# Optimization experiments

Hardware: AMD Instinct MI355X
Metric: run time of the kernel (lower is better)

Reference implementation:

```python
import jax, jax.numpy as jnp
import numpy as np

N_TASK = 50000
N_EDGE = 50000
E = 500000
F_TASK = 64
F_EDGE = 64
H = 256
OUT = 256


def _lin(key, fan_in, fan_out):
    kw, kb = jax.random.split(key)
    lim = 1.0 / np.sqrt(fan_in)
    W = jax.random.uniform(kw, (fan_in, fan_out), minval=-lim, maxval=lim, dtype=jnp.float32)
    b = jax.random.uniform(kb, (fan_out,), minval=-lim, maxval=lim, dtype=jnp.float32)
    return W, b


def setup_inputs() -> dict:
    key = jax.random.key(0)
    ks = jax.random.split(key, 20)
    inp = {}
    inp['task_features'] = jax.random.normal(ks[0], (N_TASK, F_TASK), dtype=jnp.float32)
    inp['edge_features'] = jax.random.normal(ks[1], (N_EDGE, F_EDGE), dtype=jnp.float32)
    inp['queue_edges'] = jax.random.randint(ks[2], (2, E), 0, N_TASK)
    inp['type_edges'] = jax.random.randint(ks[3], (2, E), 0, N_TASK)
    inp['affinity_edges'] = jax.random.randint(ks[4], (2, E), 0, N_TASK)  # src<num_tasks, tgt<num_edges
    inp['topology_edges'] = jax.random.randint(ks[5], (2, E), 0, N_EDGE)
    inp['te_w1'], inp['te_b1'] = _lin(ks[6], F_TASK, H)
    inp['te_w2'], inp['te_b2'] = _lin(ks[7], H, H)
    inp['ee_w1'], inp['ee_b1'] = _lin(ks[8], F_EDGE, H)
    inp['ee_w2'], inp['ee_b2'] = _lin(ks[9], H, H)
    inp['gnn_w0'], inp['gnn_b0'] = _lin(ks[10], H, H)
    inp['gnn_w1'], inp['gnn_b1'] = _lin(ks[11], H, H)
    inp['ta_w'], inp['ta_b'] = _lin(ks[12], H, H)
    inp['ea_w'], inp['ea_b'] = _lin(ks[13], H, H)
    inp['out_w1'], inp['out_b1'] = _lin(ks[14], 2 * H, H)
    inp['out_w2'], inp['out_b2'] = _lin(ks[15], H, OUT)
    return inp


def _mean_msg(src_emb, src, tgt, num_segments):
    # scatter-add messages from src nodes into tgt slots, divide by in-degree (clamped >=1)
    msgs = jax.ops.segment_sum(src_emb[src], tgt, num_segments=num_segments)
    cnt = jax.ops.segment_sum(jnp.ones_like(src, dtype=src_emb.dtype), tgt, num_segments=num_segments)
    return msgs / jnp.maximum(cnt, 1.0)[:, None]


def _forward(task_features, edge_features, queue_edges, type_edges, affinity_edges, topology_edges,
             te_w1, te_b1, te_w2, te_b2, ee_w1, ee_b1, ee_w2, ee_b2,
             gnn_w0, gnn_b0, gnn_w1, gnn_b1, ta_w, ta_b, ea_w, ea_b,
             out_w1, out_b1, out_w2, out_b2):
    relu = jax.nn.relu
    # node encoders (Linear-ReLU-Linear-ReLU)
    t = relu(relu(task_features @ te_w1 + te_b1) @ te_w2 + te_b2)   # [N_task, H]
    e = relu(relu(edge_features @ ee_w1 + ee_b1) @ ee_w2 + ee_b2)   # [N_edge, H]

    # queue convolution: messages computed ONCE from original t (torch code never updates task_embeddings in loop)
    qs, qt = queue_edges[0], queue_edges[1]
    q_msgs = jax.ops.segment_sum(t[qs], qt, num_segments=t.shape[0])
    h = t
    for W, b in ((gnn_w0, gnn_b0), (gnn_w1, gnn_b1)):
        h = relu((h + 0.5 * q_msgs) @ W + b)
    t = h

    # type convolution: mean-aggregated same-type messages
    t = t + 0.3 * _mean_msg(t, type_edges[0], type_edges[1], t.shape[0])

    # affinity convolution: bipartite task<->edge exchange (simultaneous update)
    asrc, atgt = affinity_edges[0], affinity_edges[1]
    t_msgs = jax.ops.segment_sum(e[atgt], asrc, num_segments=t.shape[0])
    t_cnt = jax.ops.segment_sum(jnp.ones((asrc.shape[0],), t.dtype), asrc, num_segments=t.shape[0])
    e_msgs = jax.ops.segment_sum(t[asrc], atgt, num_segments=e.shape[0])
    e_cnt = jax.ops.segment_sum(jnp.ones((atgt.shape[0],), e.dtype), atgt, num_segments=e.shape[0])
    t_new = t + 0.3 * t_msgs / jnp.maximum(t_cnt, 1.0)[:, None]
    e_new = e + 0.3 * e_msgs / jnp.maximum(e_cnt, 1.0)[:, None]
    t, e = t_new, e_new

    # topology convolution: edge-edge mean aggregation
    e = e + 0.3 * _mean_msg(e, topology_edges[0], topology_edges[1], e.shape[0])

    # graph-level aggregation
    t_agg = relu(jnp.mean(t, axis=0) @ ta_w + ta_b)  # [H]
    e_agg = relu(jnp.mean(e, axis=0) @ ea_w + ea_b)  # [H]
    combined = jnp.concatenate([t_agg, e_agg], axis=0)  # [2H]
    out = relu(combined @ out_w1 + out_b1) @ out_w2 + out_b2  # [OUT]
    return out


def reference(task_features, edge_features, queue_edges, type_edges, affinity_edges, topology_edges,
              te_w1, te_b1, te_w2, te_b2, ee_w1, ee_b1, ee_w2, ee_b2,
              gnn_w0, gnn_b0, gnn_w1, gnn_b1, ta_w, ta_b, ea_w, ea_b,
              out_w1, out_b1, out_w2, out_b2):
    return _forward(task_features, edge_features, queue_edges, type_edges, affinity_edges, topology_edges,
                    te_w1, te_b1, te_w2, te_b2, ee_w1, ee_b1, ee_w2, ee_b2,
                    gnn_w0, gnn_b0, gnn_w1, gnn_b1, ta_w, ta_b, ea_w, ea_b,
                    out_w1, out_b1, out_w2, out_b2)
```

## Files before the change

### kernel.cpp

```cpp
#include <hip/hip_runtime.h>

#define H 256
#define NT 50000
#define NEDGE 50000
#define NE 500000

#define NBKT 391
#define NBLK 123
#define CHUNK 4096
#define CAP 2816

typedef __attribute__((ext_vector_type(8))) short short8_t;
typedef __attribute__((ext_vector_type(4))) float f32x4;
typedef unsigned short u16;
typedef unsigned int u32;

__device__ __forceinline__ void fatomic(float* p, float v) { unsafeAtomicAdd(p, v); }

__device__ __forceinline__ float b2f(u16 v) { return __uint_as_float((u32)v << 16); }
__device__ __forceinline__ u16 f2b(float f) {
    u32 u = __float_as_uint(f);
    u += 0x7FFFu + ((u >> 16) & 1u);
    return (u16)(u >> 16);
}

__device__ __forceinline__ u32 f2fp8_1(float f) {
    u32 u = __float_as_uint(f);
    u32 s = (u >> 24) & 0x80u;
    float af = fabsf(f);
    if (af >= 448.f) return s | 0x7Eu;
    if (af < 0.015625f) {
        int m = (int)rintf(af * 512.0f);
        return s | (u32)m;
    }
    u32 au = __float_as_uint(af);
    u32 r = au + 0x7FFFFu + ((au >> 20) & 1u);
    int e = (int)(r >> 23) - 127;
    return s | (u32)(((e + 7) << 3) | ((r >> 20) & 7u));
}
__device__ __forceinline__ float fp82f_1(u32 b) {
    u32 s = (b & 0x80u) << 24;
    u32 em = b & 0x7Fu;
    float v;
    if (em >= 8) v = __uint_as_float((((em >> 3) + 120u) << 23) | ((em & 7u) << 20));
    else v = (float)em * 0.001953125f;
    return __uint_as_float(__float_as_uint(v) | s);
}
__device__ __forceinline__ u32 pk4_fp8(float a, float b, float c, float d) {
#if __has_builtin(__builtin_amdgcn_cvt_pk_fp8_f32)
    u32 r = 0;
    r = (u32)__builtin_amdgcn_cvt_pk_fp8_f32(a, b, (int)r, false);
    r = (u32)__builtin_amdgcn_cvt_pk_fp8_f32(c, d, (int)r, true);
    return r;
#else
    return f2fp8_1(a) | (f2fp8_1(b) << 8) | (f2fp8_1(c) << 16) | (f2fp8_1(d) << 24);
#endif
}
__device__ __forceinline__ float4 unpk4_fp8(u32 v) {
#if __has_builtin(__builtin_amdgcn_cvt_pk_f32_fp8)
    auto lo = __builtin_amdgcn_cvt_pk_f32_fp8(v, false);
    auto hi = __builtin_amdgcn_cvt_pk_f32_fp8(v, true);
    return make_float4(lo[0], lo[1], hi[0], hi[1]);
#else
    return make_float4(fp82f_1(v & 255u), fp82f_1((v >> 8) & 255u),
                       fp82f_1((v >> 16) & 255u), fp82f_1(v >> 24));
#endif
}

__device__ __forceinline__ const int* pick_list(
    int l, const int* a, const int* b, const int* c, const int* d, const int* e)
{ return (l == 0) ? a : (l == 1) ? b : (l == 2) ? c : (l == 3) ? d : e; }

template<int K1, bool FUSE_Q, bool XF32, bool DUAL>
__global__ __launch_bounds__(256) void fused_mlp(
    const void* __restrict__ XA, const u16* __restrict__ Q,
    const u16* __restrict__ W1hA, const u16* __restrict__ W1lA, const float* __restrict__ b1A,
    const u16* __restrict__ W2hA, const u16* __restrict__ W2lA, const float* __restrict__ b2A,
    u16* __restrict__ outA, u32* __restrict__ f8A,
    const void* __restrict__ XB,
    const u16* __restrict__ W1hB, const u16* __restrict__ W1lB, const float* __restrict__ b1B,
    const u16* __restrict__ W2hB, const u16* __restrict__ W2lB, const float* __restrict__ b2B,
    u16* __restrict__ outB, u32* __restrict__ f8B,
    int N, int nA, float s2)
{
    __shared__ u16 lds[32 * 256];
    int bid = blockIdx.x;
    const void* X = XA;
    const u16 *W1h = W1hA, *W1l = W1lA, *W2h = W2hA, *W2l = W2lA;
    const float *b1 = b1A, *b2 = b2A;
    u16* out = outA;
    u32* f8 = f8A;
    if (DUAL && bid >= nA) {
        bid -= nA; X = XB;
        W1h = W1hB; W1l = W1lB; b1 = b1B;
        W2h = W2hB; W2l = W2lB; b2 = b2B;
        out = outB; f8 = f8B;
    }
    const int m0 = bid * 32;

    constexpr int RCH = K1 / 8;
    for (int i = threadIdx.x; i < 32 * RCH; i += 256) {
        int r = i / RCH, c8 = i % RCH;
        int gr = m0 + r; if (gr >= N) gr = N - 1;
        uint4 v;
        if (XF32) {
            const float* xf = (const float*)X + (size_t)gr * K1 + c8 * 8;
            float4 a = *(const float4*)xf;
            float4 b = *(const float4*)(xf + 4);
            v.x = (u32)f2b(a.x) | ((u32)f2b(a.y) << 16);
            v.y = (u32)f2b(a.z) | ((u32)f2b(a.w) << 16);
            v.z = (u32)f2b(b.x) | ((u32)f2b(b.y) << 16);
            v.w = (u32)f2b(b.z) | ((u32)f2b(b.w) << 16);
        } else {
            v = *(const uint4*)((const u16*)X + (size_t)gr * K1 + c8 * 8);
        }
        u32 byte = (u32)(r * (K1 * 2) + c8 * 16) ^ (u32)((r & 7) << 4);
        *(uint4*)((char*)lds + byte) = v;
    }
    __syncthreads();

    const int wv = threadIdx.x >> 6, l = threadIdx.x & 63;
    const int li = l & 15, lk = l >> 4;

    f32x4 acc[2][4];
    #pragma unroll
    for (int i = 0; i < 2; i++)
        #pragma unroll
        for (int j = 0; j < 4; j++)
            acc[i][j] = (f32x4){0.f, 0.f, 0.f, 0.f};

    {
        constexpr int KS = K1 / 32;
        short8_t whc[4], wlc[4];
        #pragma unroll
        for (int ni = 0; ni < 4; ni++) {
            const size_t wi = (size_t)((wv * 4 + ni) * KS) * 64 + l;
            whc[ni] = ((const short8_t*)W1h)[wi];
            wlc[ni] = ((const short8_t*)W1l)[wi];
        }
        #pragma unroll
        for (int ks = 0; ks < KS; ks++) {
            short8_t whn[4], wln[4];
            if (ks + 1 < KS) {
                #pragma unroll
                for (int ni = 0; ni < 4; ni++) {
                    const size_t wi = (size_t)((wv * 4 + ni) * KS + ks + 1) * 64 + l;
                    whn[ni] = ((const short8_t*)W1h)[wi];
                    wln[ni] = ((const short8_t*)W1l)[wi];
                }
            }
            short8_t xb[2];
            #pragma unroll
            for (int mi = 0; mi < 2; mi++) {
                int m = mi * 16 + li;
                u32 byte = (u32)(m * (K1 * 2) + (ks * 32 + lk * 8) * 2) ^ (u32)((m & 7) << 4);
                xb[mi] = *(const short8_t*)((const char*)lds + byte);
            }
            __builtin_amdgcn_s_setprio(1);
            #pragma unroll
            for (int ni = 0; ni < 4; ni++)
                #pragma unroll
                for (int mi = 0; mi < 2; mi++) {
                    acc[mi][ni] = __builtin_amdgcn_mfma_f32_16x16x32_bf16(wlc[ni], xb[mi], acc[mi][ni], 0, 0, 0);
                    acc[mi][ni] = __builtin_amdgcn_mfma_f32_16x16x32_bf16(whc[ni], xb[mi], acc[mi][ni], 0, 0, 0);
                }
            __builtin_amdgcn_s_setprio(0);
            if (ks + 1 < KS) {
                #pragma unroll
                for (int ni = 0; ni < 4; ni++) { whc[ni] = whn[ni]; wlc[ni] = wln[ni]; }
            }
        }
    }

    __syncthreads();

    #pragma unroll
    for (int ni = 0; ni < 4; ni++) {
        int c = wv * 64 + ni * 16 + lk * 4;
        float4 b4 = *(const float4*)(b1 + c);
        #pragma unroll
        for (int mi = 0; mi < 2; mi++) {
            int m = mi * 16 + li;
            float o0 = fmaxf(acc[mi][ni][0] + b4.x, 0.f);
            float o1 = fmaxf(acc[mi][ni][1] + b4.y, 0.f);
            float o2 = fmaxf(acc[mi][ni][2] + b4.z, 0.f);
            float o3 = fmaxf(acc[mi][ni][3] + b4.w, 0.f);
            if (FUSE_Q) {
                int gm = m0 + m; if (gm >= N) gm = N - 1;
                uint2 qv = *(const uint2*)(Q + (size_t)gm * 256 + c);
                o0 = fmaf(s2, b2f((u16)(qv.x & 0xFFFF)), o0);
                o1 = fmaf(s2, b2f((u16)(qv.x >> 16)), o1);
                o2 = fmaf(s2, b2f((u16)(qv.y & 0xFFFF)), o2);
                o3 = fmaf(s2, b2f((u16)(qv.y >> 16)), o3);
            }
            u32 w0 = (u32)f2b(o0) | ((u32)f2b(o1) << 16);
            u32 w1 = (u32)f2b(o2) | ((u32)f2b(o3) << 16);
            u32 byte = (u32)(m * 512 + c * 2) ^ (u32)((m & 7) << 4);
            *(uint2*)((char*)lds + byte) = make_uint2(w0, w1);
        }
    }
    __syncthreads();

    #pragma unroll
    for (int i = 0; i < 2; i++)
        #pragma unroll
        for (int j = 0; j < 4; j++)
            acc[i][j] = (f32x4){0.f, 0.f, 0.f, 0.f};

    {
        short8_t whc[4], wlc[4];
        #pragma unroll
        for (int ni = 0; ni < 4; ni++) {
            const size_t wi = (size_t)((wv * 4 + ni) * 8) * 64 + l;
            whc[ni] = ((const short8_t*)W2h)[wi];
            wlc[ni] = ((const short8_t*)W2l)[wi];
        }
        #pragma unroll
        for (int ks = 0; ks < 8; ks++) {
            short8_t whn[4], wln[4];
            if (ks + 1 < 8) {
                #pragma unroll
                for (int ni = 0; ni < 4; ni++) {
                    const size_t wi = (size_t)((wv * 4 + ni) * 8 + ks + 1) * 64 + l;
                    whn[ni] = ((const short8_t*)W2h)[wi];
                    wln[ni] = ((const short8_t*)W2l)[wi];
                }
            }
            short8_t xb[2];
            #pragma unroll
            for (int mi = 0; mi < 2; mi++) {
                int m = mi * 16 + li;
                u32 byte = (u32)(m * 512 + (ks * 32 + lk * 8) * 2) ^ (u32)((m & 7) << 4);
                xb[mi] = *(const short8_t*)((const char*)lds + byte);
            }
            __builtin_amdgcn_s_setprio(1);
            #pragma unroll
            for (int ni = 0; ni < 4; ni++)
                #pragma unroll
                for (int mi = 0; mi < 2; mi++) {
                    acc[mi][ni] = __builtin_amdgcn_mfma_f32_16x16x32_bf16(wlc[ni], xb[mi], acc[mi][ni], 0, 0, 0);
                    acc[mi][ni] = __builtin_amdgcn_mfma_f32_16x16x32_bf16(whc[ni], xb[mi], acc[mi][ni], 0, 0, 0);
                }
            __builtin_amdgcn_s_setprio(0);
            if (ks + 1 < 8) {
                #pragma unroll
                for (int ni = 0; ni < 4; ni++) { whc[ni] = whn[ni]; wlc[ni] = wln[ni]; }
            }
        }
    }

    #pragma unroll
    for (int mi = 0; mi < 2; mi++) {
        int m = m0 + mi * 16 + li;
        if (m < N) {
            #pragma unroll
            for (int ni = 0; ni < 4; ni++) {
                int c = wv * 64 + ni * 16 + lk * 4;
                float4 b4 = *(const float4*)(b2 + c);
                float o0 = fmaxf(acc[mi][ni][0] + b4.x, 0.f);
                float o1 = fmaxf(acc[mi][ni][1] + b4.y, 0.f);
                float o2 = fmaxf(acc[mi][ni][2] + b4.z, 0.f);
                float o3 = fmaxf(acc[mi][ni][3] + b4.w, 0.f);
                u32 w0 = (u32)f2b(o0) | ((u32)f2b(o1) << 16);
                u32 w1 = (u32)f2b(o2) | ((u32)f2b(o3) << 16);
                *(uint2*)(out + (size_t)m * H + c) = make_uint2(w0, w1);
                if (f8) f8[(size_t)m * 64 + (c >> 2)] = pk4_fp8(o0, o1, o2, o3);
            }
        }
    }
}

__global__ __launch_bounds__(256) void wt_pack(
    const float* __restrict__ s0, const float* __restrict__ s1,
    const float* __restrict__ s2, const float* __restrict__ s3,
    const float* __restrict__ s4, const float* __restrict__ s5,
    u16* __restrict__ arena)
{
    const int li = blockIdx.y;
    const int K = (li == 0 || li == 4) ? 64 : 256;
    const int offs[6] = {0, 32768, 163840, 294912, 425984, 458752};
    int n = K * 256;
    int i = blockIdx.x * 256 + threadIdx.x;
    if (i >= n) return;
    const float* W = (li == 0) ? s0 : (li == 1) ? s1 : (li == 2) ? s2
                   : (li == 3) ? s3 : (li == 4) ? s4 : s5;
    u16* hi = arena + offs[li];
    u16* lo = hi + n;
    int k = i >> 8, c = i & 255;
    float u = W[i];
    u32 b = __float_as_uint(u);
    float r = u - __uint_as_float(b & 0xFFFF0000u);
    int lane = ((k >> 3) & 3) * 16 + (c & 15);
    size_t idx = ((size_t)((c >> 4) * (K >> 5) + (k >> 5)) * 64 + lane) * 8 + (k & 7);
    hi[idx] = (u16)(b >> 16);
    lo[idx] = f2b(r);
}

__global__ __launch_bounds__(256) void hist_kernel(
    const int* __restrict__ k0, const int* __restrict__ k1, const int* __restrict__ k2,
// ... 117 lines not shown
    int base = bases[l * (NBKT + 1) + b];
    int end  = bases[l * (NBKT + 1) + b + 1];
    int sz = end - base; if (sz > CAP) sz = CAP;
    int* c = csr + (size_t)l * NE;
    for (int i = t; i < sz; i += 256) seg[i] = c[base + i];
    if (t < 128) hist[t] = 0;
    __syncthreads();
    for (int i = t; i < sz; i += 256) atomicAdd(&hist[seg[i] >> 16], 1);
    __syncthreads();
    if (t < 128) scn[t] = hist[t];
    __syncthreads();
    for (int st = 1; st < 128; st <<= 1) {
        int v = 0;
        if (t < 128 && t >= st) v = scn[t - st];
        __syncthreads();
        if (t < 128) scn[t] += v;
        __syncthreads();
    }
    if (t < 128) {
        int key = b * 128 + t;
        int excl = scn[t] - hist[t];
        if (key < NT) off[l * (NT + 1) + key] = base + excl;
        hist[t] = excl;
    }
    if (b == 0 && t == 128) off[l * (NT + 1) + NT] = NE;
    __syncthreads();
    for (int i = t; i < sz; i += 256) {
        int u = seg[i];
        int p = atomicAdd(&hist[u >> 16], 1);
        c[base + p] = u & 0xFFFF;
    }
}

__global__ __launch_bounds__(256) void gather_q_f8(
    const u32* __restrict__ src, const int* __restrict__ csr,
    const int* __restrict__ off, const u16* __restrict__ baseT,
    u16* __restrict__ sumOut, u16* __restrict__ fuseOut, float s2, int N)
{
    int r = (blockIdx.x * 256 + threadIdx.x) >> 6;
    int lane = threadIdx.x & 63;
    if (r >= N) return;
    int o0 = off[r];
    int d  = off[r + 1] - o0;
    float4 acc = {0.f, 0.f, 0.f, 0.f};
    int j = 0;
    for (; j + 8 <= d; j += 8) {
        u32 w[8];
        #pragma unroll
        for (int q = 0; q < 8; q++)
            w[q] = src[(size_t)csr[o0 + j + q] * 64 + lane];
        #pragma unroll
        for (int q = 0; q < 8; q++) {
            float4 f = unpk4_fp8(w[q]);
            acc.x += f.x; acc.y += f.y; acc.z += f.z; acc.w += f.w;
        }
    }
    for (; j < d; j++) {
        float4 f = unpk4_fp8(src[(size_t)csr[o0 + j] * 64 + lane]);
        acc.x += f.x; acc.y += f.y; acc.z += f.z; acc.w += f.w;
    }
    ushort4 pk;
    pk.x = f2b(acc.x); pk.y = f2b(acc.y); pk.z = f2b(acc.z); pk.w = f2b(acc.w);
    ((ushort4*)(sumOut + (size_t)r * H))[lane] = pk;
    ushort4 b = ((const ushort4*)(baseT + (size_t)r * H))[lane];
    pk.x = f2b(fmaf(s2, acc.x, b2f(b.x)));
    pk.y = f2b(fmaf(s2, acc.y, b2f(b.y)));
    pk.z = f2b(fmaf(s2, acc.z, b2f(b.z)));
    pk.w = f2b(fmaf(s2, acc.w, b2f(b.w)));
    ((ushort4*)(fuseOut + (size_t)r * H))[lane] = pk;
}

__global__ __launch_bounds__(256) void gather_mean_f8(
    const u32* __restrict__ srcA, const int* __restrict__ csrA, const int* __restrict__ offA,
    const u16* __restrict__ baseA, u16* __restrict__ dstA, u32* __restrict__ m8A,
    const u32* __restrict__ srcB, const int* __restrict__ csrB, const int* __restrict__ offB,
    const u16* __restrict__ baseB, u16* __restrict__ dstB, u32* __restrict__ m8B,
    float alpha, int nA, int N)
{
    int bid = blockIdx.x;
    const u32* src = srcA; const int* csr = csrA; const int* off = offA;
    const u16* base = baseA; u16* dst = dstA; u32* m8 = m8A;
    if (bid >= nA) {
        bid -= nA; src = srcB; csr = csrB; off = offB; base = baseB; dst = dstB; m8 = m8B;
    }
    int r = (bid * 256 + threadIdx.x) >> 6;
    int lane = threadIdx.x & 63;
    if (r >= N) return;
    int o0 = off[r];
    int d  = off[r + 1] - o0;
    float4 acc = {0.f, 0.f, 0.f, 0.f};
    int j = 0;
    for (; j + 8 <= d; j += 8) {
        u32 w[8];
        #pragma unroll
        for (int q = 0; q < 8; q++)
            w[q] = src[(size_t)csr[o0 + j + q] * 64 + lane];
        #pragma unroll
        for (int q = 0; q < 8; q++) {
            float4 f = unpk4_fp8(w[q]);
            acc.x += f.x; acc.y += f.y; acc.z += f.z; acc.w += f.w;
        }
    }
    for (; j < d; j++) {
        float4 f = unpk4_fp8(src[(size_t)csr[o0 + j] * 64 + lane]);
        acc.x += f.x; acc.y += f.y; acc.z += f.z; acc.w += f.w;
    }
    float s = alpha / (float)max(d, 1);
    ushort4 b = ((const ushort4*)(base + (size_t)r * H))[lane];
    float o0f = fmaf(s, acc.x, b2f(b.x));
    float o1f = fmaf(s, acc.y, b2f(b.y));
    float o2f = fmaf(s, acc.z, b2f(b.z));
    float o3f = fmaf(s, acc.w, b2f(b.w));
    ushort4 pk;
    pk.x = f2b(o0f); pk.y = f2b(o1f); pk.z = f2b(o2f); pk.w = f2b(o3f);
    ((ushort4*)(dst + (size_t)r * H))[lane] = pk;
    if (m8) m8[(size_t)r * 64 + lane] = pk4_fp8(o0f, o1f, o2f, o3f);
}

__global__ __launch_bounds__(256) void colsum2(
    const u16* __restrict__ embA, float* __restrict__ accA,
    const u16* __restrict__ embB, float* __restrict__ accB, int N)
{
    const u16* emb = embA; float* acc = accA;
    int blk = blockIdx.x;
    if (blk >= 256) { blk -= 256; emb = embB; acc = accB; }
    int c = threadIdx.x;
    float s = 0.f;
    for (int r = blk; r < N; r += 256)
        s += b2f(emb[(size_t)r * H + c]);
    fatomic(&acc[c], s);
}

__global__ __launch_bounds__(256) void final_mlp(
    const float* __restrict__ sumT, const float* __restrict__ sumE,
    float invNT, float invNE,
    const float* __restrict__ ta_w, const float* __restrict__ ta_b,
    const float* __restrict__ ea_w, const float* __restrict__ ea_b,
    const float* __restrict__ ow1, const float* __restrict__ ob1,
    const float* __restrict__ ow2, const float* __restrict__ ob2,
    float* __restrict__ out)
{
    __shared__ float tm[H], em[H], comb[2 * H], hid[H];
    int t = threadIdx.x;
    tm[t] = sumT[t] * invNT;
    em[t] = sumE[t] * invNE;
    __syncthreads();
    float s = ta_b[t];
    for (int k = 0; k < H; k++) s += tm[k] * ta_w[k * H + t];
    comb[t] = fmaxf(s, 0.f);
    s = ea_b[t];
    for (int k = 0; k < H; k++) s += em[k] * ea_w[k * H + t];
    comb[H + t] = fmaxf(s, 0.f);
    __syncthreads();
    s = ob1[t];
    for (int k = 0; k < 2 * H; k++) s += comb[k] * ow1[k * H + t];
    hid[t] = fmaxf(s, 0.f);
    __syncthreads();
    s = ob2[t];
    for (int k = 0; k < H; k++) s += hid[k] * ow2[k * H + t];
    out[t] = s;
}

extern "C" void kernel_launch(void* const* d_in, const int* in_sizes, int n_in,
                              void* d_out, int out_size, void* d_ws, size_t ws_size,
                              hipStream_t stream) {
    const float* tf  = (const float*)d_in[0];
    const float* ef  = (const float*)d_in[1];
    const int*   qe  = (const int*)d_in[2];
    const int*   te  = (const int*)d_in[3];
    const int*   ae  = (const int*)d_in[4];
    const int*   pe  = (const int*)d_in[5];
    const float* te_w1 = (const float*)d_in[6];  const float* te_b1 = (const float*)d_in[7];
    const float* te_w2 = (const float*)d_in[8];  const float* te_b2 = (const float*)d_in[9];
    const float* ee_w1 = (const float*)d_in[10]; const float* ee_b1 = (const float*)d_in[11];
    const float* ee_w2 = (const float*)d_in[12]; const float* ee_b2 = (const float*)d_in[13];
    const float* gw0 = (const float*)d_in[14];   const float* gb0 = (const float*)d_in[15];
    const float* gw1 = (const float*)d_in[16];   const float* gb1 = (const float*)d_in[17];
    const float* ta_w = (const float*)d_in[18];  const float* ta_b = (const float*)d_in[19];
    const float* ea_w = (const float*)d_in[20];  const float* ea_b = (const float*)d_in[21];
    const float* ow1 = (const float*)d_in[22];   const float* ob1 = (const float*)d_in[23];
    const float* ow2 = (const float*)d_in[24];   const float* ob2 = (const float*)d_in[25];

    const size_t NB = (size_t)NT * H;
    u16* T  = (u16*)d_ws;
    u16* Bf = T + NB;
    u16* S  = Bf + NB;
    u16* F  = S + NB;
    float* sumT = (float*)(F + NB);
    float* sumE = sumT + H;
    int* off5   = (int*)(sumE + H);
    int* csr5   = off5 + 5 * (NT + 1);
    int* counts = csr5 + (size_t)5 * NE;
    int* starts = counts + (size_t)5 * NBLK * NBKT;
    int* bases  = starts + (size_t)5 * NBLK * NBKT;
    u16* arena = (u16*)(((size_t)counts + 15) & ~(size_t)15);
    u16* wt_te1_h = arena + 0;      u16* wt_te1_l = arena + 16384;
    u16* wt_te2_h = arena + 32768;  u16* wt_te2_l = arena + 98304;
    u16* wt_g0_h  = arena + 163840; u16* wt_g0_l  = arena + 229376;
    u16* wt_g1_h  = arena + 294912; u16* wt_g1_l  = arena + 360448;
    u16* wt_ee1_h = arena + 425984; u16* wt_ee1_l = arena + 442368;
    u16* wt_ee2_h = arena + 458752; u16* wt_ee2_l = arena + 524288;
    u32* M0 = (u32*)(((size_t)(bases + 5 * (NBKT + 1)) + 15) & ~(size_t)15);
    u32* M1 = M0 + NB / 4;
    u32* M2 = M1 + NB / 4;
    u32* M3 = M2 + NB / 4;
    u32* M4 = M3 + NB / 4;

    const int MGR = (NT + 31) / 32;
    const int GB = (NT * 64) / 256;

    const int *k0 = qe + NE, *k1 = te + NE, *k2 = ae,      *k3 = ae + NE, *k4 = pe + NE;
    const int *v0 = qe,      *v1 = te,      *v2 = ae + NE, *v3 = ae,      *v4 = pe;

    dim3 pg(NBLK, 5);
    hist_kernel<<<pg, 256, 0, stream>>>(k0, k1, k2, k3, k4, counts);
    scan_buckets<<<5, 256, 0, stream>>>(counts, starts, bases);
    partition_kernel<<<pg, 256, 0, stream>>>(k0, k1, k2, k3, k4, v0, v1, v2, v3, v4,
                                             starts, csr5);
    wt_pack<<<dim3(256, 6), 256, 0, stream>>>(te_w1, te_w2, gw0, gw1, ee_w1, ee_w2, arena);
    bucket_csr<<<dim3(NBKT, 5), 256, 0, stream>>>(bases, csr5, off5);

    #define LOFF(l) (off5 + (l) * (NT + 1))
    #define LCSR(l) (csr5 + (size_t)(l) * NE)

    fused_mlp<64, false, true, true><<<2 * MGR, 256, 0, stream>>>(
        tf, nullptr, wt_te1_h, wt_te1_l, te_b1, wt_te2_h, wt_te2_l, te_b2, T, M0,
        ef, wt_ee1_h, wt_ee1_l, ee_b1, wt_ee2_h, wt_ee2_l, ee_b2, Bf, M2,
        NT, MGR, 0.f);

    gather_q_f8<<<GB, 256, 0, stream>>>(M0, LCSR(0), LOFF(0), T, S, F, 0.5f, NT);

    fused_mlp<256, true, false, false><<<MGR, 256, 0, stream>>>(
        F, S, wt_g0_h, wt_g0_l, gb0, wt_g1_h, wt_g1_l, gb1, T, M1,
        nullptr, nullptr, nullptr, nullptr, nullptr, nullptr, nullptr, nullptr, nullptr,
        NT, MGR, 0.5f);

    gather_mean_f8<<<GB, 256, 0, stream>>>(
        M1, LCSR(1), LOFF(1), T, F, M3,
        M1, LCSR(1), LOFF(1), T, F, M3,
        0.3f, GB, NT);

    gather_mean_f8<<<2 * GB, 256, 0, stream>>>(
        M2, LCSR(2), LOFF(2), F, S, nullptr,
        M3, LCSR(3), LOFF(3), Bf, T, M4,
        0.3f, GB, NT);

    gather_mean_f8<<<GB, 256, 0, stream>>>(
        M4, LCSR(4), LOFF(4), T, Bf, nullptr,
        M4, LCSR(4), LOFF(4), T, Bf, nullptr,
        0.3f, GB, NT);

    hipMemsetAsync(sumT, 0, H * 4, stream);
    hipMemsetAsync(sumE, 0, H * 4, stream);
    colsum2<<<512, 256, 0, stream>>>(S, sumT, Bf, sumE, NT);
    final_mlp<<<1, 256, 0, stream>>>(sumT, sumE, 1.f / NT, 1.f / NEDGE,
                                     ta_w, ta_b, ea_w, ea_b, ow1, ob1, ow2, ob2,
                                     (float*)d_out);
}
```

Measured before the change: 465.1 us.

## Fuse queue gather into GNN MLP kernel, widen MLP tiles to 64 rows

The separate queue-edge gather kernel is folded into a new gnn_fused kernel. It aggregates fp8 neighbour messages straight into LDS and then runs both GNN linear layers, so the S and F intermediates no longer make a round trip through global memory. The fused MLP kernels now process 64 rows per block instead of 32, which doubles register accumulators and LDS use in exchange for more weight reuse. The column-sum reduction drops its memsets and atomics and writes per-block partials that final_mlp reduces serially. The risks are lower occupancy from 64 KB of LDS in gnn_fused and a serial 256-step loop in the single-block final kernel.

Measured after the change: 497.6 us. +7.0%, slower.

```diff
diff --git a/kernel.cpp b/kernel.cpp
--- a/kernel.cpp
+++ b/kernel.cpp
@@ -14,8 +14,6 @@
 typedef __attribute__((ext_vector_type(4))) float f32x4;
 typedef unsigned short u16;
 typedef unsigned int u32;
-
-__device__ __forceinline__ void fatomic(float* p, float v) { unsafeAtomicAdd(p, v); }
 
 __device__ __forceinline__ float b2f(u16 v) { return __uint_as_float((u32)v << 16); }
 __device__ __forceinline__ u16 f2b(float f) {
@@ -71,9 +69,9 @@
     int l, const int* a, const int* b, const int* c, const int* d, const int* e)
 { return (l == 0) ? a : (l == 1) ? b : (l == 2) ? c : (l == 3) ? d : e; }
 
-template<int K1, bool FUSE_Q, bool XF32, bool DUAL>
+template<int K1, bool XF32, bool DUAL>
 __global__ __launch_bounds__(256) void fused_mlp(
-    const void* __restrict__ XA, const u16* __restrict__ Q,
+    const void* __restrict__ XA,
     const u16* __restrict__ W1hA, const u16* __restrict__ W1lA, const float* __restrict__ b1A,
     const u16* __restrict__ W2hA, const u16* __restrict__ W2lA, const float* __restrict__ b2A,
     u16* __restrict__ outA, u32* __restrict__ f8A,
@@ -81,9 +79,9 @@
     const u16* __restrict__ W1hB, const u16* __restrict__ W1lB, const float* __restrict__ b1B,
     const u16* __restrict__ W2hB, const u16* __restrict__ W2lB, const float* __restrict__ b2B,
     u16* __restrict__ outB, u32* __restrict__ f8B,
-    int N, int nA, float s2)
-{
-    __shared__ u16 lds[32 * 256];
+    int N, int nA)
+{
+    __shared__ u16 lds[64 * 256];
     int bid = blockIdx.x;
     const void* X = XA;
     const u16 *W1h = W1hA, *W1l = W1lA, *W2h = W2hA, *W2l = W2lA;
@@ -96,10 +94,10 @@
         W2h = W2hB; W2l = W2lB; b2 = b2B;
         out = outB; f8 = f8B;
     }
-    const int m0 = bid * 32;
+    const int m0 = bid * 64;
 
     constexpr int RCH = K1 / 8;
-    for (int i = threadIdx.x; i < 32 * RCH; i += 256) {
+    for (int i = threadIdx.x; i < 64 * RCH; i += 256) {
         int r = i / RCH, c8 = i % RCH;
         int gr = m0 + r; if (gr >= N) gr = N - 1;
         uint4 v;
@@ -122,9 +120,9 @@
     const int wv = threadIdx.x >> 6, l = threadIdx.x & 63;
     const int li = l & 15, lk = l >> 4;
 
-    f32x4 acc[2][4];
-    #pragma unroll
-    for (int i = 0; i < 2; i++)
+    f32x4 acc[4][4];
+    #pragma unroll
+    for (int i = 0; i < 4; i++)
         #pragma unroll
         for (int j = 0; j < 4; j++)
             acc[i][j] = (f32x4){0.f, 0.f, 0.f, 0.f};
@@ -149,9 +147,9 @@
                     wln[ni] = ((const short8_t*)W1l)[wi];
                 }
             }
-            short8_t xb[2];
-            #pragma unroll
-            for (int mi = 0; mi < 2; mi++) {
+            short8_t xb[4];
+            #pragma unroll
+            for (int mi = 0; mi < 4; mi++) {
                 int m = mi * 16 + li;
                 u32 byte = (u32)(m * (K1 * 2) + (ks * 32 + lk * 8) * 2) ^ (u32)((m & 7) << 4);
                 xb[mi] = *(const short8_t*)((const char*)lds + byte);
@@ -160,7 +158,7 @@
             #pragma unroll
             for (int ni = 0; ni < 4; ni++)
                 #pragma unroll
-                for (int mi = 0; mi < 2; mi++) {
+                for (int mi = 0; mi < 4; mi++) {
                     acc[mi][ni] = __builtin_amdgcn_mfma_f32_16x16x32_bf16(wlc[ni], xb[mi], acc[mi][ni], 0, 0, 0);
                     acc[mi][ni] = __builtin_amdgcn_mfma_f32_16x16x32_bf16(whc[ni], xb[mi], acc[mi][ni], 0, 0, 0);
                 }
@@ -179,20 +177,12 @@
         int c = wv * 64 + ni * 16 + lk * 4;
         float4 b4 = *(const float4*)(b1 + c);
         #pragma unroll
-        for (int mi = 0; mi < 2; mi++) {
+        for (int mi = 0; mi < 4; mi++) {
             int m = mi * 16 + li;
             float o0 = fmaxf(acc[mi][ni][0] + b4.x, 0.f);
             float o1 = fmaxf(acc[mi][ni][1] + b4.y, 0.f);
             float o2 = fmaxf(acc[mi][ni][2] + b4.z, 0.f);
             float o3 = fmaxf(acc[mi][ni][3] + b4.w, 0.f);
-            if (FUSE_Q) {
-                int gm = m0 + m; if (gm >= N) gm = N - 1;
-                uint2 qv = *(const uint2*)(Q + (size_t)gm * 256 + c);
-                o0 = fmaf(s2, b2f((u16)(qv.x & 0xFFFF)), o0);
-                o1 = fmaf(s2, b2f((u16)(qv.x >> 16)), o1);
-                o2 = fmaf(s2, b2f((u16)(qv.y & 0xFFFF)), o2);
-                o3 = fmaf(s2, b2f((u16)(qv.y >> 16)), o3);
-            }
             u32 w0 = (u32)f2b(o0) | ((u32)f2b(o1) << 16);
             u32 w1 = (u32)f2b(o2) | ((u32)f2b(o3) << 16);
             u32 byte = (u32)(m * 512 + c * 2) ^ (u32)((m & 7) << 4);
@@ -202,7 +192,7 @@
     __syncthreads();
 
     #pragma unroll
-    for (int i = 0; i < 2; i++)
+    for (int i = 0; i < 4; i++)
         #pragma unroll
         for (int j = 0; j < 4; j++)
             acc[i][j] = (f32x4){0.f, 0.f, 0.f, 0.f};
@@ -226,9 +216,9 @@
                     wln[ni] = ((const short8_t*)W2l)[wi];
                 }
             }
-            short8_t xb[2];
-            #pragma unroll
-            for (int mi = 0; mi < 2; mi++) {
+            short8_t xb[4];
+            #pragma unroll
+            for (int mi = 0; mi < 4; mi++) {
                 int m = mi * 16 + li;
                 u32 byte = (u32)(m * 512 + (ks * 32 + lk * 8) * 2) ^ (u32)((m & 7) << 4);
                 xb[mi] = *(const short8_t*)((const char*)lds + byte);
@@ -237,7 +227,7 @@
             #pragma unroll
             for (int ni = 0; ni < 4; ni++)
                 #pragma unroll
-                for (int mi = 0; mi < 2; mi++) {
+                for (int mi = 0; mi < 4; mi++) {
                     acc[mi][ni] = __builtin_amdgcn_mfma_f32_16x16x32_bf16(wlc[ni], xb[mi], acc[mi][ni], 0, 0, 0);
                     acc[mi][ni] = __builtin_amdgcn_mfma_f32_16x16x32_bf16(whc[ni], xb[mi], acc[mi][ni], 0, 0, 0);
                 }
@@ -250,7 +240,199 @@
     }
 
     #pragma unroll
-    for (int mi = 0; mi < 2; mi++) {
+    for (int mi = 0; mi < 4; mi++) {
+        int m = m0 + mi * 16 + li;
+        if (m < N) {
+            #pragma unroll
+            for (int ni = 0; ni < 4; ni++) {
+                int c = wv * 64 + ni * 16 + lk * 4;
+                float4 b4 = *(const float4*)(b2 + c);
+                float o0 = fmaxf(acc[mi][ni][0] + b4.x, 0.f);
+                float o1 = fmaxf(acc[mi][ni][1] + b4.y, 0.f);
+                float o2 = fmaxf(acc[mi][ni][2] + b4.z, 0.f);
+                float o3 = fmaxf(acc[mi][ni][3] + b4.w, 0.f);
+                u32 w0 = (u32)f2b(o0) | ((u32)f2b(o1) << 16);
+                u32 w1 = (u32)f2b(o2) | ((u32)f2b(o3) << 16);
+                *(uint2*)(out + (size_t)m * H + c) = make_uint2(w0, w1);
+                if (f8) f8[(size_t)m * 64 + (c >> 2)] = pk4_fp8(o0, o1, o2, o3);
+            }
+        }
+    }
+}
+
+__global__ __launch_bounds__(256) void gnn_fused(
+    const u16* __restrict__ T, const u32* __restrict__ M0,
+    const int* __restrict__ csr, const int* __restrict__ off,
+    const u16* __restrict__ W1h, const u16* __restrict__ W1l, const float* __restrict__ b1,
+    const u16* __restrict__ W2h, const u16* __restrict__ W2l, const float* __restrict__ b2,
+    u16* __restrict__ out, u32* __restrict__ f8, int N)
+{
+    __shared__ u16 ldsX[64 * 256];
+    __shared__ u16 ldsS[64 * 256];
+    const int wv = threadIdx.x >> 6, l = threadIdx.x & 63;
+    const int li = l & 15, lk = l >> 4;
+    const int m0 = blockIdx.x * 64;
+
+    for (int rr = 0; rr < 16; rr++) {
+        int r = wv * 16 + rr;
+        int gr = m0 + r; if (gr >= N) gr = N - 1;
+        int o0 = off[gr];
+        int d  = off[gr + 1] - o0;
+        float4 acc = {0.f, 0.f, 0.f, 0.f};
+        int j = 0;
+        for (; j + 8 <= d; j += 8) {
+            u32 w[8];
+            #pragma unroll
+            for (int q = 0; q < 8; q++)
+                w[q] = M0[(size_t)csr[o0 + j + q] * 64 + l];
+            #pragma unroll
+            for (int q = 0; q < 8; q++) {
+                float4 f = unpk4_fp8(w[q]);
+                acc.x += f.x; acc.y += f.y; acc.z += f.z; acc.w += f.w;
+            }
+        }
+        for (; j < d; j++) {
+            float4 f = unpk4_fp8(M0[(size_t)csr[o0 + j] * 64 + l]);
+            acc.x += f.x; acc.y += f.y; acc.z += f.z; acc.w += f.w;
+        }
+        ushort4 t4 = ((const ushort4*)(T + (size_t)gr * H))[l];
+        u32 s0 = (u32)f2b(acc.x) | ((u32)f2b(acc.y) << 16);
+        u32 s1 = (u32)f2b(acc.z) | ((u32)f2b(acc.w) << 16);
+        u32 f0 = (u32)f2b(fmaf(0.5f, acc.x, b2f(t4.x)))
+               | ((u32)f2b(fmaf(0.5f, acc.y, b2f(t4.y))) << 16);
+        u32 f1 = (u32)f2b(fmaf(0.5f, acc.z, b2f(t4.z)))
+               | ((u32)f2b(fmaf(0.5f, acc.w, b2f(t4.w))) << 16);
+        u32 byte = (u32)(r * 512 + l * 8) ^ (u32)((r & 7) << 4);
+        *(uint2*)((char*)ldsX + byte) = make_uint2(f0, f1);
+        *(uint2*)((char*)ldsS + byte) = make_uint2(s0, s1);
+    }
+    __syncthreads();
+
+    f32x4 acc[4][4];
+    #pragma unroll
+    for (int i = 0; i < 4; i++)
+        #pragma unroll
+        for (int j = 0; j < 4; j++)
+            acc[i][j] = (f32x4){0.f, 0.f, 0.f, 0.f};
+
+    {
+        short8_t whc[4], wlc[4];
+        #pragma unroll
+        for (int ni = 0; ni < 4; ni++) {
+            const size_t wi = (size_t)((wv * 4 + ni) * 8) * 64 + l;
+            whc[ni] = ((const short8_t*)W1h)[wi];
+            wlc[ni] = ((const short8_t*)W1l)[wi];
+        }
+        #pragma unroll
+        for (int ks = 0; ks < 8; ks++) {
+            short8_t whn[4], wln[4];
+            if (ks + 1 < 8) {
+                #pragma unroll
+                for (int ni = 0; ni < 4; ni++) {
+                    const size_t wi = (size_t)((wv * 4 + ni) * 8 + ks + 1) * 64 + l;
+                    whn[ni] = ((const short8_t*)W1h)[wi];
+                    wln[ni] = ((const short8_t*)W1l)[wi];
+                }
+            }
+            short8_t xb[4];
+            #pragma unroll
+            for (int mi = 0; mi < 4; mi++) {
+                int m = mi * 16 + li;
+                u32 byte = (u32)(m * 512 + (ks * 32 + lk * 8) * 2) ^ (u32)((m & 7) << 4);
+                xb[mi] = *(const short8_t*)((const char*)ldsX + byte);
+            }
+            __builtin_amdgcn_s_setprio(1);
+            #pragma unroll
+            for (int ni = 0; ni < 4; ni++)
+                #pragma unroll
+                for (int mi = 0; mi < 4; mi++) {
+                    acc[mi][ni] = __builtin_amdgcn_mfma_f32_16x16x32_bf16(wlc[ni], xb[mi], acc[mi][ni], 0, 0, 0);
+                    acc[mi][ni] = __builtin_amdgcn_mfma_f32_16x16x32_bf16(whc[ni], xb[mi], acc[mi][ni], 0, 0, 0);
+                }
+            __builtin_amdgcn_s_setprio(0);
+            if (ks + 1 < 8) {
+                #pragma unroll
+                for (int ni = 0; ni < 4; ni++) { whc[ni] = whn[ni]; wlc[ni] = wln[ni]; }
+            }
+        }
+    }
+
+    __syncthreads();
+
+    #pragma unroll
+    for (int ni = 0; ni < 4; ni++) {
+        int c = wv * 64 + ni * 16 + lk * 4;
+        float4 b4 = *(const float4*)(b1 + c);
+        #pragma unroll
+        for (int mi = 0; mi < 4; mi++) {
+            int m = mi * 16 + li;
+            u32 byte = (u32)(m * 512 + c * 2) ^ (u32)((m & 7) << 4);
+            uint2 sv = *(const uint2*)((const char*)ldsS + byte);
+            float o0 = fmaxf(acc[mi][ni][0] + b4.x, 0.f);
+            float o1 = fmaxf(acc[mi][ni][1] + b4.y, 0.f);
+            float o2 = fmaxf(acc[mi][ni][2] + b4.z, 0.f);
+            float o3 = fmaxf(acc[mi][ni][3] + b4.w, 0.f);
+            o0 = fmaf(0.5f, b2f((u16)(sv.x & 0xFFFF)), o0);
+            o1 = fmaf(0.5f, b2f((u16)(sv.x >> 16)), o1);
+            o2 = fmaf(0.5f, b2f((u16)(sv.y & 0xFFFF)), o2);
+            o3 = fmaf(0.5f, b2f((u16)(sv.y >> 16)), o3);
+            u32 w0 = (u32)f2b(o0) | ((u32)f2b(o1) << 16);
+            u32 w1 = (u32)f2b(o2) | ((u32)f2b(o3) << 16);
+            *(uint2*)((char*)ldsX + byte) = make_uint2(w0, w1);
+        }
+    }
+    __syncthreads();
+
+    #pragma unroll
+    for (int i = 0; i < 4; i++)
+        #pragma unroll
+        for (int j = 0; j < 4; j++)
+            acc[i][j] = (f32x4){0.f, 0.f, 0.f, 0.f};
+
+    {
+        short8_t whc[4], wlc[4];
+        #pragma unroll
+        for (int ni = 0; ni < 4; ni++) {
+            const size_t wi = (size_t)((wv * 4 + ni) * 8) * 64 + l;
+            whc[ni] = ((const short8_t*)W2h)[wi];
+            wlc[ni] = ((const short8_t*)W2l)[wi];
+        }
+        #pragma unroll
+        for (int ks = 0; ks < 8; ks++) {
+            short8_t whn[4], wln[4];
+            if (ks + 1 < 8) {
+                #pragma unroll
+                for (int ni = 0; ni < 4; ni++) {
+                    const size_t wi = (size_t)((wv * 4 + ni) * 8 + ks + 1) * 64 + l;
+                    whn[ni] = ((const short8_t*)W2h)[wi];
+                    wln[ni] = ((const short8_t*)W2l)[wi];
+                }
+            }
+            short8_t xb[4];
+            #pragma unroll
+            for (int mi = 0; mi < 4; mi++) {
+                int m = mi * 16 + li;
+                u32 byte = (u32)(m * 512 + (ks * 32 + lk * 8) * 2) ^ (u32)((m & 7) << 4);
+                xb[mi] = *(const short8_t*)((const char*)ldsX + byte);
+            }
+            __builtin_amdgcn_s_setprio(1);
+            #pragma unroll
+            for (int ni = 0; ni < 4; ni++)
+                #pragma unroll
+                for (int mi = 0; mi < 4; mi++) {
+                    acc[mi][ni] = __builtin_amdgcn_mfma_f32_16x16x32_bf16(wlc[ni], xb[mi], acc[mi][ni], 0, 0, 0);
+                    acc[mi][ni] = __builtin_amdgcn_mfma_f32_16x16x32_bf16(whc[ni], xb[mi], acc[mi][ni], 0, 0, 0);
+                }
+            __builtin_amdgcn_s_setprio(0);
+            if (ks + 1 < 8) {
+                #pragma unroll
+                for (int ni = 0; ni < 4; ni++) { whc[ni] = whn[ni]; wlc[ni] = wln[ni]; }
+            }
+        }
+    }
+
+    #pragma unroll
+    for (int mi = 0; mi < 4; mi++) {
         int m = m0 + mi * 16 + li;
         if (m < N) {
             #pragma unroll
@@ -448,44 +630,6 @@
     }
 }
 
-__global__ __launch_bounds__(256) void gather_q_f8(
-    const u32* __restrict__ src, const int* __restrict__ csr,
-    const int* __restrict__ off, const u16* __restrict__ baseT,
-    u16* __restrict__ sumOut, u16* __restrict__ fuseOut, float s2, int N)
-{
-    int r = (blockIdx.x * 256 + threadIdx.x) >> 6;
-    int lane = threadIdx.x & 63;
-    if (r >= N) return;
-    int o0 = off[r];
-    int d  = off[r + 1] - o0;
-    float4 acc = {0.f, 0.f, 0.f, 0.f};
-    int j = 0;
-    for (; j + 8 <= d; j += 8) {
-        u32 w[8];
-        #pragma unroll
-        for (int q = 0; q < 8; q++)
-            w[q] = src[(size_t)csr[o0 + j + q] * 64 + lane];
-        #pragma unroll
-        for (int q = 0; q < 8; q++) {
-            float4 f = unpk4_fp8(w[q]);
-            acc.x += f.x; acc.y += f.y; acc.z += f.z; acc.w += f.w;
-        }
-    }
-    for (; j < d; j++) {
-        float4 f = unpk4_fp8(src[(size_t)csr[o0 + j] * 64 + lane]);
-        acc.x += f.x; acc.y += f.y; acc.z += f.z; acc.w += f.w;
-    }
-    ushort4 pk;
-    pk.x = f2b(acc.x); pk.y = f2b(acc.y); pk.z = f2b(acc.z); pk.w = f2b(acc.w);
-    ((ushort4*)(sumOut + (size_t)r * H))[lane] = pk;
-    ushort4 b = ((const ushort4*)(baseT + (size_t)r * H))[lane];
-    pk.x = f2b(fmaf(s2, acc.x, b2f(b.x)));
-    pk.y = f2b(fmaf(s2, acc.y, b2f(b.y)));
-    pk.z = f2b(fmaf(s2, acc.z, b2f(b.z)));
-    pk.w = f2b(fmaf(s2, acc.w, b2f(b.w)));
-    ((ushort4*)(fuseOut + (size_t)r * H))[lane] = pk;
-}
-
 __global__ __launch_bounds__(256) void gather_mean_f8(
     const u32* __restrict__ srcA, const int* __restrict__ csrA, const int* __restrict__ offA,
     const u16* __restrict__ baseA, u16* __restrict__ dstA, u32* __restrict__ m8A,
@@ -533,23 +677,22 @@
     if (m8) m8[(size_t)r * 64 + lane] = pk4_fp8(o0f, o1f, o2f, o3f);
 }
 
-__global__ __launch_bounds__(256) void colsum2(
-    const u16* __restrict__ embA, float* __restrict__ accA,
-    const u16* __restrict__ embB, float* __restrict__ accB, int N)
-{
-    const u16* emb = embA; float* acc = accA;
+__global__ __launch_bounds__(256) void colsum_slots(
+    const u16* __restrict__ embA, const u16* __restrict__ embB,
+    float* __restrict__ part, int N)
+{
     int blk = blockIdx.x;
-    if (blk >= 256) { blk -= 256; emb = embB; acc = accB; }
+    const u16* emb = (blk < 256) ? embA : embB;
+    int rb = blk & 255;
     int c = threadIdx.x;
     float s = 0.f;
-    for (int r = blk; r < N; r += 256)
+    for (int r = rb; r < N; r += 256)
         s += b2f(emb[(size_t)r * H + c]);
-    fatomic(&acc[c], s);
+    part[(size_t)blk * H + c] = s;
 }
 
 __global__ __launch_bounds__(256) void final_mlp(
-    const float* __restrict__ sumT, const float* __restrict__ sumE,
-    float invNT, float invNE,
+    const float* __restrict__ part, float invNT, float invNE,
     const float* __restrict__ ta_w, const float* __restrict__ ta_b,
     const float* __restrict__ ea_w, const float* __restrict__ ea_b,
     const float* __restrict__ ow1, const float* __restrict__ ob1,
@@ -558,8 +701,13 @@
 {
     __shared__ float tm[H], em[H], comb[2 * H], hid[H];
     int t = threadIdx.x;
-    tm[t] = sumT[t] * invNT;
-    em[t] = sumE[t] * invNE;
+    float st = 0.f, se = 0.f;
+    for (int b = 0; b < 256; b++) {
+        st += part[(size_t)b * H + t];
+        se += part[(size_t)(256 + b) * H + t];
+    }
+    tm[t] = st * invNT;
+    em[t] = se * invNE;
     __syncthreads();
     float s = ta_b[t];
     for (int k = 0; k < H; k++) s += tm[k] * ta_w[k * H + t];
@@ -602,9 +750,8 @@
     u16* Bf = T + NB;
     u16* S  = Bf + NB;
     u16* F  = S + NB;
-    float* sumT = (float*)(F + NB);
-    float* sumE = sumT + H;
-    int* off5   = (int*)(sumE + H);
+    float* sumpad = (float*)(F + NB);
+    int* off5   = (int*)(sumpad + 2 * H);
     int* csr5   = off5 + 5 * (NT + 1);
     int* counts = csr5 + (size_t)5 * NE;
     int* starts = counts + (size_t)5 * NBLK * NBKT;
@@ -621,8 +768,9 @@
     u32* M2 = M1 + NB / 4;
     u32* M3 = M2 + NB / 4;
     u32* M4 = M3 + NB / 4;
-
-    const int MGR = (NT + 31) / 32;
+    float* part = (float*)(M4 + NB / 4);
+
+    const int MG = (NT + 63) / 64;
     const int GB = (NT * 64) / 256;
 
     const int *k0 = qe + NE, *k1 = te + NE, *k2 = ae,      *k3 = ae + NE, *k4 = pe + NE;
@@ -639,17 +787,14 @@
     #define LOFF(l) (off5 + (l) * (NT + 1))
     #define LCSR(l) (csr5 + (size_t)(l) * NE)
 
-    fused_mlp<64, false, true, true><<<2 * MGR, 256, 0, stream>>>(
-        tf, nullptr, wt_te1_h, wt_te1_l, te_b1, wt_te2_h, wt_te2_l, te_b2, T, M0,
+    fused_mlp<64, true, true><<<2 * MG, 256, 0, stream>>>(
+        tf, wt_te1_h, wt_te1_l, te_b1, wt_te2_h, wt_te2_l, te_b2, T, M0,
         ef, wt_ee1_h, wt_ee1_l, ee_b1, wt_ee2_h, wt_ee2_l, ee_b2, Bf, M2,
-        NT, MGR, 0.f);
-
-    gather_q_f8<<<GB, 256, 0, stream>>>(M0, LCSR(0), LOFF(0), T, S, F, 0.5f, NT);
-
-    fused_mlp<256, true, false, false><<<MGR, 256, 0, stream>>>(
-        F, S, wt_g0_h, wt_g0_l, gb0, wt_g1_h, wt_g1_l, gb1, T, M1,
-        nullptr, nullptr, nullptr, nullptr, nullptr, nullptr, nullptr, nullptr, nullptr,
-        NT, MGR, 0.5f);
+        NT, MG);
+
+    gnn_fused<<<MG, 256, 0, stream>>>(
+        T, M0, LCSR(0), LOFF(0),
+        wt_g0_h, wt_g0_l, gb0, wt_g1_h, wt_g1_l, gb1, T, M1, NT);
 
     gather_mean_f8<<<GB, 256, 0, stream>>>(
         M1, LCSR(1), LOFF(1), T, F, M3,
@@ -666,10 +811,8 @@
         M4, LCSR(4), LOFF(4), T, Bf, nullptr,
         0.3f, GB, NT);
 
-    hipMemsetAsync(sumT, 0, H * 4, stream);
-    hipMemsetAsync(sumE, 0, H * 4, stream);
-    colsum2<<<512, 256, 0, stream>>>(S, sumT, Bf, sumE, NT);
-    final_mlp<<<1, 256, 0, stream>>>(sumT, sumE, 1.f / NT, 1.f / NEDGE,
+    colsum_slots<<<512, 256, 0, stream>>>(S, Bf, part, NT);
+    final_mlp<<<1, 256, 0, stream>>>(part, 1.f / NT, 1.f / NEDGE,
                                      ta_w, ta_b, ea_w, ea_b, ow1, ob1, ow2, ob2,
                                      (float*)d_out);
 }
```

## Double MLP row tile to 64, stage epilogue via LDS, drop atomic colsum

Applied to the files above, without the earlier changes.

Each fused MLP block now processes 64 rows instead of 32, so every weight fragment loaded from global memory feeds twice as many MFMAs and fewer blocks are launched. The second-layer epilogue is staged through LDS, which lets bf16 outputs and fp8 copies be written as coalesced 16-byte row stores. The column-sum kernel writes per-block partial sums instead of using atomics, and the final MLP reduces those partials, which removes the two memsets. The larger tile doubles accumulator registers and LDS use, which may lower occupancy, and halves the block count to about 782.

After: 438.7 us. -5.7%, faster.

```diff
diff --git a/kernel.cpp b/kernel.cpp
--- a/kernel.cpp
+++ b/kernel.cpp
@@ -14,8 +14,6 @@
 typedef __attribute__((ext_vector_type(4))) float f32x4;
 typedef unsigned short u16;
 typedef unsigned int u32;
-
-__device__ __forceinline__ void fatomic(float* p, float v) { unsafeAtomicAdd(p, v); }
 
 __device__ __forceinline__ float b2f(u16 v) { return __uint_as_float((u32)v << 16); }
 __device__ __forceinline__ u16 f2b(float f) {
@@ -83,7 +81,7 @@
     u16* __restrict__ outB, u32* __restrict__ f8B,
     int N, int nA, float s2)
 {
-    __shared__ u16 lds[32 * 256];
+    __shared__ u16 lds[64 * 256];
     int bid = blockIdx.x;
     const void* X = XA;
     const u16 *W1h = W1hA, *W1l = W1lA, *W2h = W2hA, *W2l = W2lA;
@@ -96,10 +94,10 @@
         W2h = W2hB; W2l = W2lB; b2 = b2B;
         out = outB; f8 = f8B;
     }
-    const int m0 = bid * 32;
+    const int m0 = bid * 64;
 
     constexpr int RCH = K1 / 8;
-    for (int i = threadIdx.x; i < 32 * RCH; i += 256) {
+    for (int i = threadIdx.x; i < 64 * RCH; i += 256) {
         int r = i / RCH, c8 = i % RCH;
         int gr = m0 + r; if (gr >= N) gr = N - 1;
         uint4 v;
@@ -122,9 +120,9 @@
     const int wv = threadIdx.x >> 6, l = threadIdx.x & 63;
     const int li = l & 15, lk = l >> 4;
 
-    f32x4 acc[2][4];
-    #pragma unroll
-    for (int i = 0; i < 2; i++)
+    f32x4 acc[4][4];
+    #pragma unroll
+    for (int i = 0; i < 4; i++)
         #pragma unroll
         for (int j = 0; j < 4; j++)
             acc[i][j] = (f32x4){0.f, 0.f, 0.f, 0.f};
@@ -149,9 +147,9 @@
                     wln[ni] = ((const short8_t*)W1l)[wi];
                 }
             }
-            short8_t xb[2];
+            short8_t xb[4];
             #pragma unroll
-            for (int mi = 0; mi < 2; mi++) {
+            for (int mi = 0; mi < 4; mi++) {
                 int m = mi * 16 + li;
                 u32 byte = (u32)(m * (K1 * 2) + (ks * 32 + lk * 8) * 2) ^ (u32)((m & 7) << 4);
                 xb[mi] = *(const short8_t*)((const char*)lds + byte);
@@ -160,7 +158,7 @@
             #pragma unroll
             for (int ni = 0; ni < 4; ni++)
                 #pragma unroll
-                for (int mi = 0; mi < 2; mi++) {
+                for (int mi = 0; mi < 4; mi++) {
                     acc[mi][ni] = __builtin_amdgcn_mfma_f32_16x16x32_bf16(wlc[ni], xb[mi], acc[mi][ni], 0, 0, 0);
                     acc[mi][ni] = __builtin_amdgcn_mfma_f32_16x16x32_bf16(whc[ni], xb[mi], acc[mi][ni], 0, 0, 0);
                 }
@@ -179,7 +177,7 @@
         int c = wv * 64 + ni * 16 + lk * 4;
         float4 b4 = *(const float4*)(b1 + c);
         #pragma unroll
-        for (int mi = 0; mi < 2; mi++) {
+        for (int mi = 0; mi < 4; mi++) {
             int m = mi * 16 + li;
             float o0 = fmaxf(acc[mi][ni][0] + b4.x, 0.f);
             float o1 = fmaxf(acc[mi][ni][1] + b4.y, 0.f);
@@ -202,7 +200,7 @@
     __syncthreads();
 
     #pragma unroll
-    for (int i = 0; i < 2; i++)
+    for (int i = 0; i < 4; i++)
         #pragma unroll
         for (int j = 0; j < 4; j++)
             acc[i][j] = (f32x4){0.f, 0.f, 0.f, 0.f};
@@ -226,9 +224,9 @@
                     wln[ni] = ((const short8_t*)W2l)[wi];
                 }
             }
-            short8_t xb[2];
+            short8_t xb[4];
             #pragma unroll
-            for (int mi = 0; mi < 2; mi++) {
+            for (int mi = 0; mi < 4; mi++) {
                 int m = mi * 16 + li;
                 u32 byte = (u32)(m * 512 + (ks * 32 + lk * 8) * 2) ^ (u32)((m & 7) << 4);
                 xb[mi] = *(const short8_t*)((const char*)lds + byte);
@@ -237,7 +235,7 @@
             #pragma unroll
             for (int ni = 0; ni < 4; ni++)
                 #pragma unroll
-                for (int mi = 0; mi < 2; mi++) {
+                for (int mi = 0; mi < 4; mi++) {
                     acc[mi][ni] = __builtin_amdgcn_mfma_f32_16x16x32_bf16(wlc[ni], xb[mi], acc[mi][ni], 0, 0, 0);
                     acc[mi][ni] = __builtin_amdgcn_mfma_f32_16x16x32_bf16(whc[ni], xb[mi], acc[mi][ni], 0, 0, 0);
                 }
@@ -249,22 +247,38 @@
         }
     }
 
-    #pragma unroll
-    for (int mi = 0; mi < 2; mi++) {
-        int m = m0 + mi * 16 + li;
+    __syncthreads();
+    #pragma unroll
+    for (int ni = 0; ni < 4; ni++) {
+        int c = wv * 64 + ni * 16 + lk * 4;
+        float4 b4 = *(const float4*)(b2 + c);
+        #pragma unroll
+        for (int mi = 0; mi < 4; mi++) {
+            int m = mi * 16 + li;
+            float o0 = fmaxf(acc[mi][ni][0] + b4.x, 0.f);
+            float o1 = fmaxf(acc[mi][ni][1] + b4.y, 0.f);
+            float o2 = fmaxf(acc[mi][ni][2] + b4.z, 0.f);
+            float o3 = fmaxf(acc[mi][ni][3] + b4.w, 0.f);
+            u32 w0 = (u32)f2b(o0) | ((u32)f2b(o1) << 16);
+            u32 w1 = (u32)f2b(o2) | ((u32)f2b(o3) << 16);
+            u32 byte = (u32)(m * 512 + c * 2) ^ (u32)((m & 7) << 4);
+            *(uint2*)((char*)lds + byte) = make_uint2(w0, w1);
+        }
+    }
+    __syncthreads();
+    for (int i = threadIdx.x; i < 64 * 32; i += 256) {
+        int r = i >> 5, c8 = i & 31;
+        int m = m0 + r;
         if (m < N) {
-            #pragma unroll
-            for (int ni = 0; ni < 4; ni++) {
-                int c = wv * 64 + ni * 16 + lk * 4;
-                float4 b4 = *(const float4*)(b2 + c);
-                float o0 = fmaxf(acc[mi][ni][0] + b4.x, 0.f);
-                float o1 = fmaxf(acc[mi][ni][1] + b4.y, 0.f);
-                float o2 = fmaxf(acc[mi][ni][2] + b4.z, 0.f);
-                float o3 = fmaxf(acc[mi][ni][3] + b4.w, 0.f);
-                u32 w0 = (u32)f2b(o0) | ((u32)f2b(o1) << 16);
-                u32 w1 = (u32)f2b(o2) | ((u32)f2b(o3) << 16);
-                *(uint2*)(out + (size_t)m * H + c) = make_uint2(w0, w1);
-                if (f8) f8[(size_t)m * 64 + (c >> 2)] = pk4_fp8(o0, o1, o2, o3);
+            u32 byte = (u32)(r * 512 + c8 * 16) ^ (u32)((r & 7) << 4);
+            uint4 v = *(const uint4*)((const char*)lds + byte);
+            *(uint4*)(out + (size_t)m * H + c8 * 8) = v;
+            if (f8) {
+                u32 p0 = pk4_fp8(b2f((u16)(v.x & 0xFFFF)), b2f((u16)(v.x >> 16)),
+                                 b2f((u16)(v.y & 0xFFFF)), b2f((u16)(v.y >> 16)));
+                u32 p1 = pk4_fp8(b2f((u16)(v.z & 0xFFFF)), b2f((u16)(v.z >> 16)),
+                                 b2f((u16)(v.w & 0xFFFF)), b2f((u16)(v.w >> 16)));
+                *(uint2*)(f8 + (size_t)m * 64 + c8 * 2) = make_uint2(p0, p1);
             }
         }
     }
@@ -533,23 +547,22 @@
     if (m8) m8[(size_t)r * 64 + lane] = pk4_fp8(o0f, o1f, o2f, o3f);
 }
 
-__global__ __launch_bounds__(256) void colsum2(
-    const u16* __restrict__ embA, float* __restrict__ accA,
-    const u16* __restrict__ embB, float* __restrict__ accB, int N)
-{
-    const u16* emb = embA; float* acc = accA;
+__global__ __launch_bounds__(256) void colsum_slots(
+    const u16* __restrict__ embA, const u16* __restrict__ embB,
+    float* __restrict__ part, int N)
+{
     int blk = blockIdx.x;
-    if (blk >= 256) { blk -= 256; emb = embB; acc = accB; }
+    const u16* emb = (blk < 256) ? embA : embB;
+    int rb = blk & 255;
     int c = threadIdx.x;
     float s = 0.f;
-    for (int r = blk; r < N; r += 256)
+    for (int r = rb; r < N; r += 256)
         s += b2f(emb[(size_t)r * H + c]);
-    fatomic(&acc[c], s);
+    part[(size_t)blk * H + c] = s;
 }
 
 __global__ __launch_bounds__(256) void final_mlp(
-    const float* __restrict__ sumT, const float* __restrict__ sumE,
-    float invNT, float invNE,
+    const float* __restrict__ part, float invNT, float invNE,
     const float* __restrict__ ta_w, const float* __restrict__ ta_b,
     const float* __restrict__ ea_w, const float* __restrict__ ea_b,
     const float* __restrict__ ow1, const float* __restrict__ ob1,
@@ -558,8 +571,13 @@
 {
     __shared__ float tm[H], em[H], comb[2 * H], hid[H];
     int t = threadIdx.x;
-    tm[t] = sumT[t] * invNT;
-    em[t] = sumE[t] * invNE;
+    float st = 0.f, se = 0.f;
+    for (int b = 0; b < 256; b++) {
+        st += part[(size_t)b * H + t];
+        se += part[(size_t)(256 + b) * H + t];
+    }
+    tm[t] = st * invNT;
+    em[t] = se * invNE;
     __syncthreads();
     float s = ta_b[t];
     for (int k = 0; k < H; k++) s += tm[k] * ta_w[k * H + t];
@@ -602,9 +620,8 @@
     u16* Bf = T + NB;
     u16* S  = Bf + NB;
     u16* F  = S + NB;
-    float* sumT = (float*)(F + NB);
-    float* sumE = sumT + H;
-    int* off5   = (int*)(sumE + H);
+    float* sumpad = (float*)(F + NB);
+    int* off5   = (int*)(sumpad + 2 * H);
     int* csr5   = off5 + 5 * (NT + 1);
     int* counts = csr5 + (size_t)5 * NE;
     int* starts = counts + (size_t)5 * NBLK * NBKT;
@@ -621,8 +638,9 @@
     u32* M2 = M1 + NB / 4;
     u32* M3 = M2 + NB / 4;
     u32* M4 = M3 + NB / 4;
-
-    const int MGR = (NT + 31) / 32;
+    float* part = (float*)(M4 + NB / 4);
+
+    const int MG = (NT + 63) / 64;
     const int GB = (NT * 64) / 256;
 
     const int *k0 = qe + NE, *k1 = te + NE, *k2 = ae,      *k3 = ae + NE, *k4 = pe + NE;
@@ -639,17 +657,17 @@
     #define LOFF(l) (off5 + (l) * (NT + 1))
     #define LCSR(l) (csr5 + (size_t)(l) * NE)
 
-    fused_mlp<64, false, true, true><<<2 * MGR, 256, 0, stream>>>(
+    fused_mlp<64, false, true, true><<<2 * MG, 256, 0, stream>>>(
         tf, nullptr, wt_te1_h, wt_te1_l, te_b1, wt_te2_h, wt_te2_l, te_b2, T, M0,
         ef, wt_ee1_h, wt_ee1_l, ee_b1, wt_ee2_h, wt_ee2_l, ee_b2, Bf, M2,
-        NT, MGR, 0.f);
+        NT, MG, 0.f);
 
     gather_q_f8<<<GB, 256, 0, stream>>>(M0, LCSR(0), LOFF(0), T, S, F, 0.5f, NT);
 
-    fused_mlp<256, true, false, false><<<MGR, 256, 0, stream>>>(
+    fused_mlp<256, true, false, false><<<MG, 256, 0, stream>>>(
         F, S, wt_g0_h, wt_g0_l, gb0, wt_g1_h, wt_g1_l, gb1, T, M1,
         nullptr, nullptr, nullptr, nullptr, nullptr, nullptr, nullptr, nullptr, nullptr,
-        NT, MGR, 0.5f);
+        NT, MG, 0.5f);
 
     gather_mean_f8<<<GB, 256, 0, stream>>>(
         M1, LCSR(1), LOFF(1), T, F, M3,
@@ -666,10 +684,8 @@
         M4, LCSR(4), LOFF(4), T, Bf, nullptr,
         0.3f, GB, NT);
 
-    hipMemsetAsync(sumT, 0, H * 4, stream);
-    hipMemsetAsync(sumE, 0, H * 4, stream);
-    colsum2<<<512, 256, 0, stream>>>(S, sumT, Bf, sumE, NT);
-    final_mlp<<<1, 256, 0, stream>>>(sumT, sumE, 1.f / NT, 1.f / NEDGE,
+    colsum_slots<<<512, 256, 0, stream>>>(S, Bf, part, NT);
+    final_mlp<<<1, 256, 0, stream>>>(part, 1.f / NT, 1.f / NEDGE,
                                      ta_w, ta_b, ea_w, ea_b, ow1, ob1, ow2, ob2,
                                      (float*)d_out);
 }
```
